# Kernel optimization log

Hardware: AMD Instinct MI355X
Metric: run time of the kernel (lower is better)

## Reference

```python
import jax, jax.numpy as jnp
import numpy as np

P_FACTOR = 3.0   # config['p_factor']
EPS = 1e-12      # torch F.normalize eps

def _l2_normalize(x):
    return x / jnp.maximum(jnp.linalg.norm(x, axis=-1, keepdims=True), EPS)

def _l1_normalize(x):
    return x / jnp.maximum(jnp.sum(jnp.abs(x), axis=-1, keepdims=True), EPS)

def setup_inputs() -> dict:
    key = jax.random.key(0)
    k = jax.random.split(key, 6)
    B, N_EX, D_IN, D_FEAT, N_LAB, D_CLS = 4096, 16384, 1024, 256, 28, 64
    features = jax.random.normal(k[0], (B, D_IN), jnp.float32)
    labels = jax.random.uniform(k[1], (B, N_LAB), jnp.float32)            # BCE targets in [0,1]
    ex_features = jax.random.normal(k[2], (N_EX, D_IN), jnp.float32)
    ex_classes = jax.random.uniform(k[3], (N_EX, N_LAB), jnp.float32)     # class memberships
    g_w = jax.random.normal(k[4], (D_FEAT, D_IN), jnp.float32) * 0.02     # Linear(in=1024,out=256,bias=False)
    class_reps = jax.random.uniform(k[5], (N_LAB, D_CLS), jnp.float32) * 2.0 - 1.0  # rand*2-1
    return {"features": features, "labels": labels, "ex_features": ex_features,
            "ex_classes": ex_classes, "g_w": g_w, "class_reps": class_reps}

def reference(features, labels, ex_features, ex_classes, g_w, class_reps):
    # g projection (use_g=True, no bias)
    f = features @ g_w.T          # [B, D_FEAT]
    ef = ex_features @ g_w.T      # [N_EX, D_FEAT]
    # exemplar class representations: L1-normalized memberships @ class_reps
    ex_class_reps = _l1_normalize(ex_classes) @ class_reps   # [N_EX, D_CLS]
    # cosine similarity between queries and exemplars
    s = _l2_normalize(f) @ _l2_normalize(ef).T               # [B, N_EX]
    # power-sign activation then L1 normalize over exemplars
    a = _l1_normalize(jnp.sign(s) * jnp.abs(s) ** P_FACTOR)  # [B, N_EX]
    # weighted exemplar aggregation
    echo = a @ ex_class_reps                                  # [B, D_CLS]
    # negative euclidean distances to class representations (cdist)
    diff = echo[:, None, :] - class_reps[None, :, :]          # [B, N_LAB, D_CLS]
    neg_dists = -jnp.sqrt(jnp.sum(diff * diff, axis=-1))      # [B, N_LAB]
    # BCEWithLogitsLoss (mean reduction)
    loss = jnp.mean(-(labels * jax.nn.log_sigmoid(neg_dists)
                      + (1.0 - labels) * jax.nn.log_sigmoid(-neg_dists)))
    return (loss, neg_dists)
```

## Files before the change

kernel.cpp:

```cpp
#include <hip/hip_runtime.h>


typedef __bf16 bf16x8 __attribute__((ext_vector_type(8)));
typedef __bf16 bf16x4 __attribute__((ext_vector_type(4)));
typedef float  f32x4  __attribute__((ext_vector_type(4)));

__device__ __forceinline__ f32x4 f4zero() { f32x4 z = {0.f, 0.f, 0.f, 0.f}; return z; }

__device__ __forceinline__ f32x4 mfma16(bf16x8 a, bf16x8 b, f32x4 c) {
  return __builtin_amdgcn_mfma_f32_16x16x32_bf16(a, b, c, 0, 0, 0);
}

__device__ __forceinline__ bf16x8 load8f(const float* p) {
  f32x4 a = *(const f32x4*)p;
  f32x4 b = *(const f32x4*)(p + 4);
  bf16x8 r;
  r[0] = (__bf16)a[0]; r[1] = (__bf16)a[1]; r[2] = (__bf16)a[2]; r[3] = (__bf16)a[3];
  r[4] = (__bf16)b[0]; r[5] = (__bf16)b[1]; r[6] = (__bf16)b[2]; r[7] = (__bf16)b[3];
  return r;
}

__device__ __forceinline__ bf16x8 cvt2(f32x4 a, f32x4 b) {
  bf16x8 r;
  r[0] = (__bf16)a[0]; r[1] = (__bf16)a[1]; r[2] = (__bf16)a[2]; r[3] = (__bf16)a[3];
  r[4] = (__bf16)b[0]; r[5] = (__bf16)b[1]; r[6] = (__bf16)b[2]; r[7] = (__bf16)b[3];
  return r;
}

__device__ __forceinline__ void async16(const void* g, void* l) {
  __builtin_amdgcn_global_load_lds(
      (const __attribute__((address_space(1))) unsigned int*)g,
      (__attribute__((address_space(3))) unsigned int*)l, 16, 0, 0);
}

__device__ __forceinline__ void bar_lgkm() {
  asm volatile("s_waitcnt lgkmcnt(0)" ::: "memory");
  __builtin_amdgcn_s_barrier();
}
__device__ __forceinline__ void bar_all() {
  asm volatile("s_waitcnt vmcnt(0) lgkmcnt(0)" ::: "memory");
  __builtin_amdgcn_s_barrier();
}

__global__ void fill_sentinel(float* __restrict__ out, int n) {
  for (int i = blockIdx.x * 256 + threadIdx.x; i < n; i += gridDim.x * 256) out[i] = -1.0f;
}

__global__ void prep(const float* __restrict__ exc, __bf16* __restrict__ vT,
                     const float* __restrict__ W, __bf16* __restrict__ W2,
                     float* __restrict__ zp, int zn) {
  const int b = blockIdx.x, tid = threadIdx.x;
  if (b < 64) {
    int e = b * 256 + tid;
    float m[28];
    float s = 0.f;
#pragma unroll
    for (int j = 0; j < 28; j++) {
      m[j] = exc[(size_t)e * 28 + j];
      s += fabsf(m[j]);
    }
    float inv = 1.0f / fmaxf(s, 1e-12f);
#pragma unroll
    for (int j = 0; j < 28; j++) vT[(size_t)j * 16384 + e] = (__bf16)(m[j] * inv);
#pragma unroll
    for (int j = 28; j < 32; j++) vT[(size_t)j * 16384 + e] = (__bf16)0.0f;
  } else if (b < 192) {
    int i = (b - 64) * 256 + tid;
    *(bf16x8*)(W2 + (size_t)i * 8) = load8f(W + (size_t)i * 8);
  } else {
    for (int i = (b - 192) * 256 + tid; i < zn; i += (gridDim.x - 192) * 256) zp[i] = 0.f;
  }
}

__global__ __launch_bounds__(256, 3)
void proj_l2norm(const float* __restrict__ Xa, const float* __restrict__ Xb,
                 const __bf16* __restrict__ W2,
                 __bf16* __restrict__ Pa, __bf16* __restrict__ Pb) {
  __shared__ __align__(16) __bf16 Xs[2][32 * 136];
  __shared__ float nrmW[4 * 32];
  __shared__ float invn[32];

  const int tid = threadIdx.x;
  const int w = tid >> 6, lane = tid & 63;
  const int quad = lane >> 4, l15 = lane & 15;
  const int srow = tid >> 4, sc = tid & 15;

  const float* X;
  __bf16* P;
  int row0;
  if (blockIdx.x < 512) { X = Xa; P = Pa; row0 = blockIdx.x * 32; }
  else                  { X = Xb; P = Pb; row0 = (blockIdx.x - 512) * 32; }

  const float* xp0 = X + (size_t)(row0 + srow) * 1024 + sc * 8;
  const float* xp1 = xp0 + (size_t)16 * 1024;

  *(bf16x8*)(&Xs[0][srow * 136 + sc * 8])        = load8f(xp0);
  *(bf16x8*)(&Xs[0][(srow + 16) * 136 + sc * 8]) = load8f(xp1);

  f32x4 acc[2][4];
#pragma unroll
  for (int i = 0; i < 2; i++)
#pragma unroll
    for (int j = 0; j < 4; j++) acc[i][j] = f4zero();

  const __bf16* wstrip = W2 + (size_t)(w * 64) * 1024;

  __syncthreads();

  int cur = 0;
  for (int kb = 0; kb < 8; kb++) {
    const int nxt = cur ^ 1;
    f32x4 p00, p01, p10, p11;
    if (kb < 7) {
      const float* q0 = xp0 + (kb + 1) * 128;
      const float* q1 = xp1 + (kb + 1) * 128;
      p00 = *(const f32x4*)q0; p01 = *(const f32x4*)(q0 + 4);
      p10 = *(const f32x4*)q1; p11 = *(const f32x4*)(q1 + 4);
    }
    const __bf16* wk = wstrip + kb * 128;
#pragma unroll
    for (int ksub = 0; ksub < 4; ksub++) {
      bf16x8 af[2], bfr[4];
#pragma unroll
      for (int mb = 0; mb < 2; mb++)
        af[mb] = *(bf16x8*)(&Xs[cur][(mb * 16 + l15) * 136 + ksub * 32 + quad * 8]);
#pragma unroll
      for (int nb = 0; nb < 4; nb++)
        bfr[nb] = *(const bf16x8*)(wk + (size_t)(nb * 16 + l15) * 1024 + ksub * 32 + quad * 8);
#pragma unroll
      for (int mb = 0; mb < 2; mb++)
#pragma unroll
        for (int nb = 0; nb < 4; nb++)
          acc[mb][nb] = mfma16(af[mb], bfr[nb], acc[mb][nb]);
    }
    if (kb < 7) {
      *(bf16x8*)(&Xs[nxt][srow * 136 + sc * 8])        = cvt2(p00, p01);
      *(bf16x8*)(&Xs[nxt][(srow + 16) * 136 + sc * 8]) = cvt2(p10, p11);
    }
    __syncthreads();
    cur = nxt;
  }

  float part[2][4];
#pragma unroll
  for (int mb = 0; mb < 2; mb++)
#pragma unroll
    for (int r = 0; r < 4; r++) {
      float s = 0.f;
#pragma unroll
      for (int nb = 0; nb < 4; nb++) { float v = acc[mb][nb][r]; s += v * v; }
      part[mb][r] = s;
    }
#pragma unroll
  for (int m = 1; m < 16; m <<= 1)
#pragma unroll
    for (int mb = 0; mb < 2; mb++)
#pragma unroll
      for (int r = 0; r < 4; r++) part[mb][r] += __shfl_xor(part[mb][r], m, 64);

  if (l15 == 0) {
#pragma unroll
    for (int mb = 0; mb < 2; mb++)
#pragma unroll
      for (int r = 0; r < 4; r++)
        nrmW[w * 32 + mb * 16 + quad * 4 + r] = part[mb][r];
  }
  __syncthreads();
  if (tid < 32) {
    float s = nrmW[tid] + nrmW[32 + tid] + nrmW[64 + tid] + nrmW[96 + tid];
    invn[tid] = 1.0f / fmaxf(sqrtf(s), 1e-12f);
  }
  __syncthreads();
#pragma unroll
  for (int mb = 0; mb < 2; mb++)
#pragma unroll
    for (int nb = 0; nb < 4; nb++)
#pragma unroll
      for (int r = 0; r < 4; r++) {
        int row = mb * 16 + quad * 4 + r;
        int col = w * 64 + nb * 16 + l15;
        P[(size_t)(row0 + row) * 256 + col] = (__bf16)(acc[mb][nb][r] * invn[row]);
      }
}

__global__ __launch_bounds__(256, 2)
void fused_sim(const __bf16* __restrict__ fn, const __bf16* __restrict__ efn,
               const __bf16* __restrict__ vTg,
               float* __restrict__ tT, float* __restrict__ r_acc) {
  __shared__ __align__(16) __bf16 Ks[64 * 256];
  __shared__ __align__(16) __bf16 Vs[2][32 * 64];
  __shared__ __align__(16) __bf16 Us[128 * 72];

  const int tid = threadIdx.x, w = tid >> 6, lane = tid & 63;
  const int quad = lane >> 4, l15 = lane & 15;
  const int wy = w >> 1, wx = w & 1;
  const int swk = l15 & 7;
  const int chunk = blockIdx.x & 15, mtile = blockIdx.x >> 4;
  const int q0 = mtile * 128;
  const int e_base = chunk * 1024;

  int koff[8];
#pragma unroll
  for (int rep = 0; rep < 8; rep++) {
    int idx = rep * 256 + tid;
    int row = idx >> 5;
    int c5  = (idx & 31) ^ (row & 7);
    koff[rep] = row * 256 + c5 * 8;
  }
  const int vrow = tid >> 3;
  const int vcs  = (tid & 7) ^ (vrow & 7);
  const size_t vsrc0 = (size_t)vrow * 16384 + e_base + vcs * 8;

  {
    const __bf16* src = efn + (size_t)e_base * 256;
#pragma unroll
    for (int rep = 0; rep < 8; rep++) async16(src + koff[rep], Ks + (rep * 256 + tid) * 8);
    async16(vTg + vsrc0, &Vs[0][tid * 8]);
  }

  bf16x8 qf[8][4];
#pragma unroll
  for (int ks = 0; ks < 8; ks++)
#pragma unroll
    for (int nb = 0; nb < 4; nb++)
      qf[ks][nb] = *(const bf16x8*)(fn + (size_t)(q0 + wx * 64 + nb * 16 + l15) * 256 +
                                    ks * 32 + quad * 8);

  float r_part[4] = {0.f, 0.f, 0.f, 0.f};
  f32x4 accp[2][2];
#pragma unroll
  for (int a = 0; a < 2; a++)
#pragma unroll
    for (int b = 0; b < 2; b++) accp[a][b] = f4zero();

  bar_all();

  int cur = 0;
  for (int t = 0; t < 16; t++) {
    f32x4 accs[2][4];
#pragma unroll
    for (int a = 0; a < 2; a++)
#pragma unroll
      for (int b = 0; b < 4; b++) accs[a][b] = f4zero();
#pragma unroll
    for (int ks = 0; ks < 8; ks++) {
      bf16x8 af[2];
#pragma unroll
      for (int mb = 0; mb < 2; mb++)
        af[mb] = *(bf16x8*)(Ks + (wy * 32 + mb * 16 + l15) * 256 +
                            ((ks * 4 + quad) ^ swk) * 8);
#pragma unroll
      for (int mb = 0; mb < 2; mb++)
#pragma unroll
        for (int nb = 0; nb < 4; nb++)
          accs[mb][nb] = mfma16(af[mb], qf[ks][nb], accs[mb][nb]);
    }

    bar_lgkm();

    if (t < 15) {
      const __bf16* src = efn + (size_t)(e_base + (t + 1) * 64) * 256;
#pragma unroll
      for (int rep = 0; rep < 8; rep++)
        async16(src + koff[rep], Ks + (rep * 256 + tid) * 8);
      async16(vTg + vsrc0 + (t + 1) * 64, &Vs[cur ^ 1][tid * 8]);
    }

#pragma unroll
    for (int mb = 0; mb < 2; mb++) {
      const int eo = wy * 32 + mb * 16 + quad * 4;
#pragma unroll
      for (int nb = 0; nb < 4; nb++) {
        const int q = wx * 64 + nb * 16 + l15;
        bf16x4 pk;
#pragma unroll
        for (int r = 0; r < 4; r++) {
          float s = accs[mb][nb][r];
          __bf16 ub = (__bf16)(s * s * s);
          pk[r] = ub;
          r_part[nb] += fabsf((float)ub);
        }
        *(bf16x4*)(Us + q * 72 + eo) = pk;
      }
    }

    bar_lgkm();

#pragma unroll
    for (int ks = 0; ks < 2; ks++) {
      bf16x8 vf[2], uf[2];
#pragma unroll
      for (int cb = 0; cb < 2; cb++)
        vf[cb] = *(bf16x8*)(&Vs[cur][(cb * 16 + l15) * 64 + ((ks * 4 + quad) ^ swk) * 8]);
#pragma unroll
      for (int qb = 0; qb < 2; qb++)
        uf[qb] = *(bf16x8*)(Us + (w * 32 + qb * 16 + l15) * 72 + ks * 32 + quad * 8);
#pragma unroll
      for (int cb = 0; cb < 2; cb++)
#pragma unroll
        for (int qb = 0; qb < 2; qb++)
          accp[cb][qb] = mfma16(vf[cb], uf[qb], accp[cb][qb]);
    }

    bar_all();
    cur ^= 1;
  }

#pragma unroll
  for (int nb = 0; nb < 4; nb++) {
    float v = r_part[nb];
    v += __shfl_xor(v, 16, 64);
    v += __shfl_xor(v, 32, 64);
    if (quad == 0) atomicAdd(&r_acc[q0 + wx * 64 + nb * 16 + l15], v);
  }
#pragma unroll
  for (int cb = 0; cb < 2; cb++)
#pragma unroll
    for (int qb = 0; qb < 2; qb++)
#pragma unroll
      for (int r = 0; r < 4; r++)
        atomicAdd(&tT[(size_t)(cb * 16 + quad * 4 + r) * 4096 + q0 + w * 32 + qb * 16 + l15],
                  accp[cb][qb][r]);
}

__global__ __launch_bounds__(256, 4)
void finalize(const float* __restrict__ tT, const float* __restrict__ r_acc,
              const float* __restrict__ creps, const float* __restrict__ labels,
              float* __restrict__ loss_acc, float* __restrict__ out) {
  __shared__ __align__(16) float cr[28 * 64];
  __shared__ float wsum[4];
  const int tid = threadIdx.x, w = tid >> 6, lane = tid & 63;
  for (int i = tid; i < 28 * 64; i += 256) cr[i] = creps[i];
  __syncthreads();

  const int q = blockIdx.x * 4 + w;
  float tval = 0.f;
  if (lane < 28) tval = tT[(size_t)lane * 4096 + q];
  tval *= 1.0f / fmaxf(r_acc[q], 1e-12f);

  float echo = 0.f;
#pragma unroll
  for (int j = 0; j < 28; j++)
    echo = fmaf(__shfl(tval, j, 64), cr[j * 64 + lane], echo);

  float dj = 0.f;
#pragma unroll
  for (int j = 0; j < 28; j++) {
    float df = echo - cr[j * 64 + lane];
    float d2 = df * df;
#pragma unroll
    for (int m = 1; m < 64; m <<= 1) d2 += __shfl_xor(d2, m, 64);
    if (lane == j) dj = sqrtf(d2);
  }

  float lsum = 0.f;
  if (lane < 28) {
    out[1 + (size_t)q * 28 + lane] = -dj;
    float y = labels[(size_t)q * 28 + lane];
    lsum = fmaf(y, dj, log1pf(expf(-dj)));
  }
#pragma unroll
  for (int m = 1; m < 64; m <<= 1) lsum += __shfl_xor(lsum, m, 64);
  if (lane == 0) wsum[w] = lsum;
  __syncthreads();
  if (tid == 0) {
    atomicAdd(loss_acc, wsum[0] + wsum[1] + wsum[2] + wsum[3]);
    __threadfence();
    unsigned* cnt = (unsigned*)(loss_acc + 1);
    unsigned old = atomicAdd(cnt, 1u);
    if (old == gridDim.x - 1) {
      float total = atomicAdd(loss_acc, 0.0f);
      out[0] = total * (1.0f / 114688.0f);
    }
  }
}

extern "C" void kernel_launch(void* const* d_in, const int* in_sizes, int n_in,
                              void* d_out, int out_size, void* d_ws, size_t ws_size,
                              hipStream_t stream) {
  const float* features = nullptr;
  const float* labels   = nullptr;
  const float* ex_feat  = nullptr;
  const float* ex_cls   = nullptr;
  const float* g_w      = nullptr;
  const float* creps    = nullptr;
  for (int i = 0; i < n_in; i++) {
    switch (in_sizes[i]) {
      case 4194304:  features = (const float*)d_in[i]; break;
      case 114688:   labels   = (const float*)d_in[i]; break;
      case 16777216: ex_feat  = (const float*)d_in[i]; break;
      case 458752:   ex_cls   = (const float*)d_in[i]; break;
      case 262144:   g_w      = (const float*)d_in[i]; break;
      case 1792:     creps    = (const float*)d_in[i]; break;
      default: break;
    }
  }
  float* out = (float*)d_out;

  if (!features || !labels || !ex_feat || !ex_cls || !g_w || !creps ||
      ws_size < (16ull << 20)) {
    fill_sentinel<<<256, 256, 0, stream>>>(out, out_size);
    return;
  }

  char* ws = (char*)d_ws;
  __bf16* f_n   = (__bf16*)(ws);
  __bf16* ef_n  = (__bf16*)(ws + (2ull << 20));
  __bf16* vT    = (__bf16*)(ws + (10ull << 20));
  float*  tT    = (float*) (ws + (11ull << 20));
  float*  r_acc = tT + 32 * 4096;
  float*  lossp = r_acc + 4096;
  __bf16* W2    = (__bf16*)(ws + (12ull << 20));

  prep<<<720, 256, 0, stream>>>(ex_cls, vT, g_w, W2, tT, 32 * 4096 + 4096 + 2);

  proj_l2norm<<<640, 256, 0, stream>>>(ex_feat, features, W2, ef_n, f_n);
  fused_sim<<<512, 256, 0, stream>>>(f_n, ef_n, vT, tT, r_acc);
  finalize<<<1024, 256, 0, stream>>>(tT, r_acc, creps, labels, lossp, out);
}
```

Baseline: 240.3 us.

## Register double-buffer W fragments and halve K tile in projection kernel

The projection GEMM now steps through K in chunks of 64 instead of 128. W fragments are prefetched into two register buffers (wA/wB) one step ahead, alongside the X tile prefetch, so global weight loads are issued before the MFMAs that consume them rather than loaded in line. The shared X tile shrinks with the smaller K chunk, and the loop uses a bar_lgkm barrier helper. This is meant to hide global load latency in the projection stage. The cost is more barriers per K and higher register pressure, which could hurt occupancy under launch_bounds(256,3).

```diff
diff --git a/kernel.cpp b/kernel.cpp
--- a/kernel.cpp
+++ b/kernel.cpp
@@ -72,18 +72,44 @@
   }
 }
 
+__device__ __forceinline__ void loadw8(bf16x8* dst, const __bf16* wbase, int kel,
+                                       int l15, int quad) {
+#pragma unroll
+  for (int i = 0; i < 8; i++) {
+    const int ksub = i >> 2, nb = i & 3;
+    dst[i] = *(const bf16x8*)(wbase + (size_t)(nb * 16 + l15) * 1024 + kel +
+                              ksub * 32 + quad * 8);
+  }
+}
+
+__device__ __forceinline__ void comp8(const __bf16* Xbuf, const bf16x8* wr,
+                                      f32x4 acc[2][4], int l15, int quad) {
+#pragma unroll
+  for (int ksub = 0; ksub < 2; ksub++) {
+    bf16x8 af[2];
+#pragma unroll
+    for (int mb = 0; mb < 2; mb++)
+      af[mb] = *(const bf16x8*)(Xbuf + (mb * 16 + l15) * 72 + ksub * 32 + quad * 8);
+#pragma unroll
+    for (int mb = 0; mb < 2; mb++)
+#pragma unroll
+      for (int nb = 0; nb < 4; nb++)
+        acc[mb][nb] = mfma16(af[mb], wr[ksub * 4 + nb], acc[mb][nb]);
+  }
+}
+
 __global__ __launch_bounds__(256, 3)
 void proj_l2norm(const float* __restrict__ Xa, const float* __restrict__ Xb,
                  const __bf16* __restrict__ W2,
                  __bf16* __restrict__ Pa, __bf16* __restrict__ Pb) {
-  __shared__ __align__(16) __bf16 Xs[2][32 * 136];
+  __shared__ __align__(16) __bf16 Xs[2][32 * 72];
   __shared__ float nrmW[4 * 32];
   __shared__ float invn[32];
 
   const int tid = threadIdx.x;
   const int w = tid >> 6, lane = tid & 63;
   const int quad = lane >> 4, l15 = lane & 15;
-  const int srow = tid >> 4, sc = tid & 15;
+  const int xrow = tid >> 3, xc8 = tid & 7;
 
   const float* X;
   __bf16* P;
@@ -91,11 +117,8 @@
   if (blockIdx.x < 512) { X = Xa; P = Pa; row0 = blockIdx.x * 32; }
   else                  { X = Xb; P = Pb; row0 = (blockIdx.x - 512) * 32; }
 
-  const float* xp0 = X + (size_t)(row0 + srow) * 1024 + sc * 8;
-  const float* xp1 = xp0 + (size_t)16 * 1024;
-
-  *(bf16x8*)(&Xs[0][srow * 136 + sc * 8])        = load8f(xp0);
-  *(bf16x8*)(&Xs[0][(srow + 16) * 136 + sc * 8]) = load8f(xp1);
+  const float* xsrc = X + (size_t)(row0 + xrow) * 1024 + xc8 * 8;
+  const __bf16* wbase = W2 + (size_t)(w * 64) * 1024;
 
   f32x4 acc[2][4];
 #pragma unroll
@@ -103,42 +126,35 @@
 #pragma unroll
     for (int j = 0; j < 4; j++) acc[i][j] = f4zero();
 
-  const __bf16* wstrip = W2 + (size_t)(w * 64) * 1024;
-
-  __syncthreads();
-
-  int cur = 0;
-  for (int kb = 0; kb < 8; kb++) {
-    const int nxt = cur ^ 1;
-    f32x4 p00, p01, p10, p11;
-    if (kb < 7) {
-      const float* q0 = xp0 + (kb + 1) * 128;
-      const float* q1 = xp1 + (kb + 1) * 128;
-      p00 = *(const f32x4*)q0; p01 = *(const f32x4*)(q0 + 4);
-      p10 = *(const f32x4*)q1; p11 = *(const f32x4*)(q1 + 4);
-    }
-    const __bf16* wk = wstrip + kb * 128;
-#pragma unroll
-    for (int ksub = 0; ksub < 4; ksub++) {
-      bf16x8 af[2], bfr[4];
-#pragma unroll
-      for (int mb = 0; mb < 2; mb++)
-        af[mb] = *(bf16x8*)(&Xs[cur][(mb * 16 + l15) * 136 + ksub * 32 + quad * 8]);
-#pragma unroll
-      for (int nb = 0; nb < 4; nb++)
-        bfr[nb] = *(const bf16x8*)(wk + (size_t)(nb * 16 + l15) * 1024 + ksub * 32 + quad * 8);
-#pragma unroll
-      for (int mb = 0; mb < 2; mb++)
-#pragma unroll
-        for (int nb = 0; nb < 4; nb++)
-          acc[mb][nb] = mfma16(af[mb], bfr[nb], acc[mb][nb]);
-    }
-    if (kb < 7) {
-      *(bf16x8*)(&Xs[nxt][srow * 136 + sc * 8])        = cvt2(p00, p01);
-      *(bf16x8*)(&Xs[nxt][(srow + 16) * 136 + sc * 8]) = cvt2(p10, p11);
-    }
-    __syncthreads();
-    cur = nxt;
+  bf16x8 wA[8], wB[8];
+
+  *(bf16x8*)(&Xs[0][xrow * 72 + xc8 * 8]) = load8f(xsrc);
+  loadw8(wA, wbase, 0, l15, quad);
+  bar_lgkm();
+
+  for (int kb = 0; kb < 16; kb += 2) {
+    f32x4 xp0, xp1;
+    {
+      loadw8(wB, wbase, (kb + 1) * 64, l15, quad);
+      const float* xp = xsrc + (kb + 1) * 64;
+      xp0 = *(const f32x4*)xp;
+      xp1 = *(const f32x4*)(xp + 4);
+    }
+    comp8(&Xs[0][0], wA, acc, l15, quad);
+    *(bf16x8*)(&Xs[1][xrow * 72 + xc8 * 8]) = cvt2(xp0, xp1);
+    bar_lgkm();
+
+    if (kb + 2 < 16) {
+      loadw8(wA, wbase, (kb + 2) * 64, l15, quad);
+      const float* xq = xsrc + (kb + 2) * 64;
+      xp0 = *(const f32x4*)xq;
+      xp1 = *(const f32x4*)(xq + 4);
+    }
+    comp8(&Xs[1][0], wB, acc, l15, quad);
+    if (kb + 2 < 16) {
+      *(bf16x8*)(&Xs[0][xrow * 72 + xc8 * 8]) = cvt2(xp0, xp1);
+    }
+    bar_lgkm();
   }
 
   float part[2][4];
```

After: 236.9 us. No clear change (-1.4%).

## Restructure projection kernel to register-resident X rows with split-K wave pairs

Applied to the files above, without the earlier changes.

The projection+L2-normalize kernel no longer stages X through double-buffered LDS. Each wave now holds a 16-row slice of X in registers and computes all 256 output columns over half of K. Wave pairs combine their partial sums through LDS, and one wave of each pair then normalizes and stores. This drops the per-k-block LDS staging and barriers and gives each wave a wider N tile. In exchange, register pressure rises (16 bf16x8 fragments plus 16 accumulators), occupancy is lowered to 2 blocks, and W is read straight from global memory by every wave.

```diff
diff --git a/kernel.cpp b/kernel.cpp
--- a/kernel.cpp
+++ b/kernel.cpp
@@ -14,13 +14,6 @@
 __device__ __forceinline__ bf16x8 load8f(const float* p) {
   f32x4 a = *(const f32x4*)p;
   f32x4 b = *(const f32x4*)(p + 4);
-  bf16x8 r;
-  r[0] = (__bf16)a[0]; r[1] = (__bf16)a[1]; r[2] = (__bf16)a[2]; r[3] = (__bf16)a[3];
-  r[4] = (__bf16)b[0]; r[5] = (__bf16)b[1]; r[6] = (__bf16)b[2]; r[7] = (__bf16)b[3];
-  return r;
-}
-
-__device__ __forceinline__ bf16x8 cvt2(f32x4 a, f32x4 b) {
   bf16x8 r;
   r[0] = (__bf16)a[0]; r[1] = (__bf16)a[1]; r[2] = (__bf16)a[2]; r[3] = (__bf16)a[3];
   r[4] = (__bf16)b[0]; r[5] = (__bf16)b[1]; r[6] = (__bf16)b[2]; r[7] = (__bf16)b[3];
@@ -72,115 +65,82 @@
   }
 }
 
-__global__ __launch_bounds__(256, 3)
+__global__ __launch_bounds__(256, 2)
 void proj_l2norm(const float* __restrict__ Xa, const float* __restrict__ Xb,
                  const __bf16* __restrict__ W2,
                  __bf16* __restrict__ Pa, __bf16* __restrict__ Pb) {
-  __shared__ __align__(16) __bf16 Xs[2][32 * 136];
-  __shared__ float nrmW[4 * 32];
-  __shared__ float invn[32];
+  __shared__ __align__(16) float cpart[2][16 * 260];
 
   const int tid = threadIdx.x;
   const int w = tid >> 6, lane = tid & 63;
   const int quad = lane >> 4, l15 = lane & 15;
-  const int srow = tid >> 4, sc = tid & 15;
+  const int pair = w >> 1, kh = w & 1;
 
   const float* X;
   __bf16* P;
   int row0;
   if (blockIdx.x < 512) { X = Xa; P = Pa; row0 = blockIdx.x * 32; }
   else                  { X = Xb; P = Pb; row0 = (blockIdx.x - 512) * 32; }
-
-  const float* xp0 = X + (size_t)(row0 + srow) * 1024 + sc * 8;
-  const float* xp1 = xp0 + (size_t)16 * 1024;
-
-  *(bf16x8*)(&Xs[0][srow * 136 + sc * 8])        = load8f(xp0);
-  *(bf16x8*)(&Xs[0][(srow + 16) * 136 + sc * 8]) = load8f(xp1);
-
-  f32x4 acc[2][4];
-#pragma unroll
-  for (int i = 0; i < 2; i++)
-#pragma unroll
-    for (int j = 0; j < 4; j++) acc[i][j] = f4zero();
-
-  const __bf16* wstrip = W2 + (size_t)(w * 64) * 1024;
-
+  row0 += pair * 16;
+
+  bf16x8 xf[16];
+  const float* xrow = X + (size_t)(row0 + l15) * 1024 + kh * 512 + quad * 8;
+#pragma unroll
+  for (int kw = 0; kw < 16; kw++) xf[kw] = load8f(xrow + kw * 32);
+
+  f32x4 acc[16];
+#pragma unroll
+  for (int i = 0; i < 16; i++) acc[i] = f4zero();
+
+  const __bf16* wb = W2 + (size_t)l15 * 1024 + kh * 512 + quad * 8;
+#pragma unroll 2
+  for (int kw = 0; kw < 16; kw++) {
+#pragma unroll
+    for (int nb = 0; nb < 16; nb++) {
+      bf16x8 bfr = *(const bf16x8*)(wb + (size_t)nb * 16384 + kw * 32);
+      acc[nb] = mfma16(xf[kw], bfr, acc[nb]);
+    }
+  }
+
+  if (kh == 0) {
+#pragma unroll
+    for (int nb = 0; nb < 16; nb++)
+#pragma unroll
+      for (int r = 0; r < 4; r++)
+        cpart[pair][(quad * 4 + r) * 260 + nb * 16 + l15] = acc[nb][r];
+  }
   __syncthreads();
-
-  int cur = 0;
-  for (int kb = 0; kb < 8; kb++) {
-    const int nxt = cur ^ 1;
-    f32x4 p00, p01, p10, p11;
-    if (kb < 7) {
-      const float* q0 = xp0 + (kb + 1) * 128;
-      const float* q1 = xp1 + (kb + 1) * 128;
-      p00 = *(const f32x4*)q0; p01 = *(const f32x4*)(q0 + 4);
-      p10 = *(const f32x4*)q1; p11 = *(const f32x4*)(q1 + 4);
-    }
-    const __bf16* wk = wstrip + kb * 128;
-#pragma unroll
-    for (int ksub = 0; ksub < 4; ksub++) {
-      bf16x8 af[2], bfr[4];
-#pragma unroll
-      for (int mb = 0; mb < 2; mb++)
-        af[mb] = *(bf16x8*)(&Xs[cur][(mb * 16 + l15) * 136 + ksub * 32 + quad * 8]);
-#pragma unroll
-      for (int nb = 0; nb < 4; nb++)
-        bfr[nb] = *(const bf16x8*)(wk + (size_t)(nb * 16 + l15) * 1024 + ksub * 32 + quad * 8);
-#pragma unroll
-      for (int mb = 0; mb < 2; mb++)
-#pragma unroll
-        for (int nb = 0; nb < 4; nb++)
-          acc[mb][nb] = mfma16(af[mb], bfr[nb], acc[mb][nb]);
-    }
-    if (kb < 7) {
-      *(bf16x8*)(&Xs[nxt][srow * 136 + sc * 8])        = cvt2(p00, p01);
-      *(bf16x8*)(&Xs[nxt][(srow + 16) * 136 + sc * 8]) = cvt2(p10, p11);
-    }
-    __syncthreads();
-    cur = nxt;
-  }
-
-  float part[2][4];
-#pragma unroll
-  for (int mb = 0; mb < 2; mb++)
+  if (kh == 1) {
+#pragma unroll
+    for (int nb = 0; nb < 16; nb++)
+#pragma unroll
+      for (int r = 0; r < 4; r++)
+        acc[nb][r] += cpart[pair][(quad * 4 + r) * 260 + nb * 16 + l15];
+
+    float part[4];
 #pragma unroll
     for (int r = 0; r < 4; r++) {
       float s = 0.f;
 #pragma unroll
-      for (int nb = 0; nb < 4; nb++) { float v = acc[mb][nb][r]; s += v * v; }
-      part[mb][r] = s;
-    }
-#pragma unroll
-  for (int m = 1; m < 16; m <<= 1)
-#pragma unroll
-    for (int mb = 0; mb < 2; mb++)
-#pragma unroll
-      for (int r = 0; r < 4; r++) part[mb][r] += __shfl_xor(part[mb][r], m, 64);
-
-  if (l15 == 0) {
-#pragma unroll
-    for (int mb = 0; mb < 2; mb++)
+      for (int nb = 0; nb < 16; nb++) { float v = acc[nb][r]; s = fmaf(v, v, s); }
+      part[r] = s;
+    }
+#pragma unroll
+    for (int m = 1; m < 16; m <<= 1)
+#pragma unroll
+      for (int r = 0; r < 4; r++) part[r] += __shfl_xor(part[r], m, 64);
+
+    float inv[4];
+#pragma unroll
+    for (int r = 0; r < 4; r++) inv[r] = 1.0f / fmaxf(sqrtf(part[r]), 1e-12f);
+
+#pragma unroll
+    for (int nb = 0; nb < 16; nb++)
 #pragma unroll
       for (int r = 0; r < 4; r++)
-        nrmW[w * 32 + mb * 16 + quad * 4 + r] = part[mb][r];
-  }
-  __syncthreads();
-  if (tid < 32) {
-    float s = nrmW[tid] + nrmW[32 + tid] + nrmW[64 + tid] + nrmW[96 + tid];
-    invn[tid] = 1.0f / fmaxf(sqrtf(s), 1e-12f);
-  }
-  __syncthreads();
-#pragma unroll
-  for (int mb = 0; mb < 2; mb++)
-#pragma unroll
-    for (int nb = 0; nb < 4; nb++)
-#pragma unroll
-      for (int r = 0; r < 4; r++) {
-        int row = mb * 16 + quad * 4 + r;
-        int col = w * 64 + nb * 16 + l15;
-        P[(size_t)(row0 + row) * 256 + col] = (__bf16)(acc[mb][nb][r] * invn[row]);
-      }
+        P[(size_t)(row0 + quad * 4 + r) * 256 + nb * 16 + l15] =
+            (__bf16)(acc[nb][r] * inv[r]);
+  }
 }
 
 __global__ __launch_bounds__(256, 2)
```

New measurement: 300.0 us. 1.25x slower.
